# Kernel tuning notes

Measured on AMD Instinct MI355X. Metric: run time of the kernel, lower is better.

## Reference

```python
import jax, jax.numpy as jnp
import numpy as np
import math

NUM_HEADS = 8
HEAD_DIM = 64
SEQ = 128
EPS = 1e-6


def _rel_pos_bucket(rel_pos, num_buckets=32, max_dist=128):
    # bidirectional T5 bucketing
    n = -rel_pos
    num_buckets //= 2  # 16
    ret = (n < 0).astype(jnp.int32) * num_buckets
    n = jnp.abs(n)
    max_exact = num_buckets // 2  # 8
    is_small = n < max_exact
    nf = jnp.maximum(n, 1).astype(jnp.float32)  # guard log(0); masked by is_small
    val_if_large = max_exact + (
        jnp.log(nf / max_exact) / math.log(max_dist / max_exact) * (num_buckets - max_exact)
    ).astype(jnp.int32)
    val_if_large = jnp.minimum(val_if_large, num_buckets - 1)
    return ret + jnp.where(is_small, n, val_if_large)


def setup_inputs() -> dict:
    key = jax.random.key(0)
    ks = jax.random.split(key, 8)
    d = 512
    return {
        "x": jax.random.randint(ks[0], (1, SEQ), 0, 32128),
        "x_len": jax.random.randint(ks[1], (1,), 64, SEQ + 1),
        "embed": jax.random.normal(ks[2], (32128, d), jnp.float32) * 0.02,
        "scale": jnp.ones((d,), jnp.float32),
        "rel_bias_w": jax.random.normal(ks[3], (NUM_HEADS, 32), jnp.float32) * 0.02,
        "qw": jax.random.normal(ks[4], (d, d), jnp.float32) * 0.02,
        "kw": jax.random.normal(ks[5], (d, d), jnp.float32) * 0.02,
        "vw": jax.random.normal(ks[6], (d, d), jnp.float32) * 0.02,
    }


def reference(x, x_len, embed, scale, rel_bias_w, qw, kw, vw):
    B, S = x.shape  # (1, 128)
    H, D = NUM_HEADS, HEAD_DIM

    # embedding gather + RMSNorm + length mask
    h = embed[x]  # [B,S,512]
    var = jnp.mean(jnp.square(h), axis=-1, keepdims=True)
    h = h * jax.lax.rsqrt(var + EPS) * scale
    mask = (jnp.arange(S) < x_len[:, None]).astype(h.dtype)  # [B,S]
    h = h * mask[..., None]

    # relative-position bias gather [H,S,S]
    pos = jnp.arange(S, dtype=jnp.int32)
    rp_bucket = _rel_pos_bucket(pos[:, None] - pos[None, :])  # [S,S]
    rel_bias = rel_bias_w[:, rp_bucket]  # [H,S,S]
    rel_bias = rel_bias + (1.0 - mask[..., None]) * -1e9  # B==1 broadcast

    def split_heads(e):
        # [B,S,512] -> [B*H,S,D]
        return e.reshape(B, S, H, D).transpose(0, 2, 1, 3).reshape(B * H, S, D)

    q = split_heads(h @ qw)
    k = split_heads(h @ kw)
    v = split_heads(h @ vw)

    attn_weights = jnp.einsum("hqd,hkd->hqk", q, k)  # [B*H,S,S]
    attn_weights = attn_weights + jnp.transpose(rel_bias, (0, 2, 1))
    attn_probs = jax.nn.softmax(attn_weights, axis=-1)
    attn_output = jnp.einsum("hqk,hkd->hqd", attn_probs, v)  # [B*H,S,D]
    return (rel_bias, attn_weights, attn_output)
```

## Files before the change

kernel.cpp:

```cpp
#include <hip/hip_runtime.h>

#define SEQL 128
#define DM   512
#define NH   8
#define HD   64
#define MAGIC 0x13371337

typedef unsigned short ushort_t;
typedef unsigned int   uint_t;
typedef __attribute__((ext_vector_type(8))) __bf16 bf16x8;
typedef __attribute__((ext_vector_type(4))) float  f32x4;

__device__ __forceinline__ ushort_t f2bf(float f) {
    uint_t u = __float_as_uint(f);
    u += 0x7fffu + ((u >> 16) & 1u);
    return (ushort_t)(u >> 16);
}

__device__ __forceinline__ int bucket_of_delta(int d) {
    int n = d;
    int ret = 0;
    if (n < 0) { ret = 16; n = -n; }
    if (n < 8) return ret + n;
    float nf = (float)n;
    int vil = 8 + (int)((logf(nf * 0.125f) / logf(16.0f)) * 8.0f);
    vil = vil < 15 ? vil : 15;
    return ret + vil;
}

__global__ __launch_bounds__(256) void k_all(
    const int* __restrict__ x, const int* __restrict__ xlen,
    const float* __restrict__ embed, const float* __restrict__ scale,
    const float* __restrict__ rbw,
    const float* __restrict__ qw, const float* __restrict__ kw,
    const float* __restrict__ vw,
    float* __restrict__ q, float* __restrict__ k, float* __restrict__ v,
    int* __restrict__ flags,
    float* __restrict__ relb, float* __restrict__ aw, float* __restrict__ ao) {
    __shared__ char smem[49152];
    const int b = blockIdx.x, t = threadIdx.x;
    const int xl = xlen[0];

    if (b < 96) {
        ushort_t* Ash = (ushort_t*)smem;
        ushort_t* Bsh = (ushort_t*)(smem + 32768);
        const int xb = b & 7, yb = (b >> 3) & 3, zb = b >> 5;
        const int n0 = xb * 64, m0 = yb * 32;
        const float* __restrict__ W = (zb == 0) ? qw : (zb == 1) ? kw : vw;
        float* __restrict__ O       = (zb == 0) ? q  : (zb == 1) ? k  : v;

        const int nloc = t & 63, khq = t >> 6;
        const float* __restrict__ wcol = W + n0 + nloc;
        float rc[16];
#pragma unroll
        for (int i = 0; i < 16; ++i) rc[i] = wcol[(size_t)(khq * 16 + i) * DM];

        const int lane7 = t & 7, mloc = t >> 3;
        const int m = m0 + mloc;
        const int tok = x[m];
        const float4* er4 = reinterpret_cast<const float4*>(embed + (size_t)tok * DM);
        float4 va[8], vb8[8];
#pragma unroll
        for (int j = 0; j < 8; ++j) {
            va[j]  = er4[lane7 * 2 + j * 16];
            vb8[j] = er4[lane7 * 2 + j * 16 + 1];
        }
        float ss = 0.0f;
#pragma unroll
        for (int j = 0; j < 8; ++j) {
            ss += va[j].x * va[j].x + va[j].y * va[j].y + va[j].z * va[j].z + va[j].w * va[j].w;
            ss += vb8[j].x * vb8[j].x + vb8[j].y * vb8[j].y + vb8[j].z * vb8[j].z + vb8[j].w * vb8[j].w;
        }
        ss += __shfl_xor(ss, 1);
        ss += __shfl_xor(ss, 2);
        ss += __shfl_xor(ss, 4);
        float inv = rsqrtf(ss * (1.0f / DM) + 1e-6f);
        if (m >= xl) inv = 0.0f;
        const float4* sc4 = reinterpret_cast<const float4*>(scale);
#pragma unroll
        for (int j = 0; j < 8; ++j) {
            const int c = lane7 + 8 * j;
            const float4 s0 = sc4[c * 2];
            const float4 s1 = sc4[c * 2 + 1];
            ushort_t u[8];
            u[0] = f2bf(va[j].x * inv * s0.x);  u[1] = f2bf(va[j].y * inv * s0.y);
            u[2] = f2bf(va[j].z * inv * s0.z);  u[3] = f2bf(va[j].w * inv * s0.w);
            u[4] = f2bf(vb8[j].x * inv * s1.x); u[5] = f2bf(vb8[j].y * inv * s1.y);
            u[6] = f2bf(vb8[j].z * inv * s1.z); u[7] = f2bf(vb8[j].w * inv * s1.w);
            *reinterpret_cast<uint4*>((char*)Ash + mloc * 1024 + ((c ^ (mloc & 7)) << 4)) =
                *reinterpret_cast<const uint4*>(u);
        }

        {
            ushort_t u[16];
#pragma unroll
            for (int i = 0; i < 16; ++i) u[i] = f2bf(rc[i]);
            char* base = (char*)Bsh + nloc * 128;
            *reinterpret_cast<uint4*>(base + (((khq * 2 + 0) ^ (nloc & 7)) << 4)) =
                *reinterpret_cast<const uint4*>(&u[0]);
            *reinterpret_cast<uint4*>(base + (((khq * 2 + 1) ^ (nloc & 7)) << 4)) =
                *reinterpret_cast<const uint4*>(&u[8]);
        }
#pragma unroll
        for (int i = 0; i < 16; ++i) rc[i] = wcol[(size_t)(64 + khq * 16 + i) * DM];
        __syncthreads();

        const int wn = t >> 6, lane = t & 63;
        const int g = lane >> 4, l15 = lane & 15;
        f32x4 acc[2] = {};

#pragma unroll
        for (int it = 0; it < 8; ++it) {
            bf16x8 af[2][2], bfr[2];
#pragma unroll
            for (int fm = 0; fm < 2; ++fm) {
                const int ml = fm * 16 + l15;
#pragma unroll
                for (int kh = 0; kh < 2; ++kh) {
                    const int c = it * 8 + kh * 4 + g;
                    af[fm][kh] = *reinterpret_cast<const bf16x8*>(
                        (const char*)Ash + ml * 1024 + ((c ^ (ml & 7)) << 4));
                }
            }
            {
                const int nl = wn * 16 + l15;
#pragma unroll
                for (int kh = 0; kh < 2; ++kh) {
                    const int c = kh * 4 + g;
                    bfr[kh] = *reinterpret_cast<const bf16x8*>(
                        (const char*)Bsh + (it & 1) * 8192 + nl * 128 + ((c ^ (nl & 7)) << 4));
                }
            }
#pragma unroll
            for (int kh = 0; kh < 2; ++kh)
#pragma unroll
                for (int fm = 0; fm < 2; ++fm)
                    acc[fm] = __builtin_amdgcn_mfma_f32_16x16x32_bf16(
                        af[fm][kh], bfr[kh], acc[fm], 0, 0, 0);

            if (it < 7) {
                ushort_t u[16];
#pragma unroll
                for (int i = 0; i < 16; ++i) u[i] = f2bf(rc[i]);
                char* base = (char*)Bsh + ((it + 1) & 1) * 8192 + nloc * 128;
                *reinterpret_cast<uint4*>(base + (((khq * 2 + 0) ^ (nloc & 7)) << 4)) =
                    *reinterpret_cast<const uint4*>(&u[0]);
                *reinterpret_cast<uint4*>(base + (((khq * 2 + 1) ^ (nloc & 7)) << 4)) =
                    *reinterpret_cast<const uint4*>(&u[8]);
                if (it < 6) {
#pragma unroll
                    for (int i = 0; i < 16; ++i)
                        rc[i] = wcol[(size_t)((it + 2) * 64 + khq * 16 + i) * DM];
                }
            }
            __syncthreads();
        }

        {
            const int nn = n0 + wn * 16 + l15;
            float* od = O + ((size_t)(nn >> 6) * SEQL) * HD + (nn & 63);
#pragma unroll
            for (int fm = 0; fm < 2; ++fm)
#pragma unroll
                for (int r = 0; r < 4; ++r) {
                    const int mm = m0 + fm * 16 + g * 4 + r;
                    od[(size_t)mm * HD] = acc[fm][r];
                }
        }
        __syncthreads();
        if (t == 0)
            __hip_atomic_store(&flags[b], MAGIC, __ATOMIC_RELEASE,
                               __HIP_MEMORY_SCOPE_AGENT);
    } else if (b < 352) {
        float (*Ks)[HD + 4] = (float(*)[HD + 4])smem;
        float (*ps)[SEQL]   = (float(*)[SEQL])(smem + 34816);
        float* tbl          = (float*)(smem + 36864);
        const int a = b - 96, hh = a >> 5, q0 = (a & 31) * 4;

        if (t < 255) tbl[t] = rbw[hh * 32 + bucket_of_delta(t - 127)];

        if (t < 9) {
            const int fi = (t == 0) ? ((q0 >> 5) * 8 + hh)
                         : (t < 5)  ? (32 + (t - 1) * 8 + hh)
                                    : (64 + (t - 5) * 8 + hh);
            while (__hip_atomic_load(&flags[fi], __ATOMIC_RELAXED,
                                     __HIP_MEMORY_SCOPE_AGENT) != MAGIC)
                __builtin_amdgcn_s_sleep(2);
        }
        __syncthreads();
        if (t == 0)
            (void)__hip_atomic_load(&flags[0], __ATOMIC_ACQUIRE,
                                    __HIP_MEMORY_SCOPE_AGENT);
        __syncthreads();

        const float* __restrict__ kb = k + (size_t)hh * SEQL * HD;
        const float* __restrict__ vb = v + (size_t)hh * SEQL * HD;
        const float4* kb4 = reinterpret_cast<const float4*>(kb);
#pragma unroll
        for (int i = 0; i < 8; ++i) {
            const int e4 = t + i * 256;
            *reinterpret_cast<float4*>(&Ks[e4 >> 4][(e4 & 15) * 4]) = kb4[e4];
        }
        const int w = t >> 6, lane = t & 63;
        const int qi = q0 + w;
        const float4* qrow4 = reinterpret_cast<const float4*>(q + (size_t)(hh * SEQL + qi) * HD);
        float4 qr[16];
#pragma unroll
        for (int i = 0; i < 16; ++i) qr[i] = qrow4[i];
        __syncthreads();

        float lg[2];
#pragma unroll
        for (int p = 0; p < 2; ++p) {
            const int kk = lane + p * 64;
            float acc = 0.0f;
#pragma unroll
            for (int d4 = 0; d4 < 16; ++d4) {
                const float4 kv = *reinterpret_cast<const float4*>(&Ks[kk][d4 * 4]);
                acc += qr[d4].x * kv.x + qr[d4].y * kv.y + qr[d4].z * kv.z + qr[d4].w * kv.w;
            }
            float bias = tbl[qi - kk + 127];
            if (kk >= xl) bias += -1e9f;
            acc += bias;
            lg[p] = acc;
            aw[(size_t)hh * SEQL * SEQL + qi * SEQL + kk] = acc;
        }
        float mx = fmaxf(lg[0], lg[1]);
#pragma unroll
        for (int o = 32; o > 0; o >>= 1) mx = fmaxf(mx, __shfl_xor(mx, o));
        const float e0 = expf(lg[0] - mx);
        const float e1 = expf(lg[1] - mx);
        float sm = e0 + e1;
#pragma unroll
        for (int o = 32; o > 0; o >>= 1) sm += __shfl_xor(sm, o);
        const float inv = 1.0f / sm;
        ps[w][lane]      = e0 * inv;
        ps[w][lane + 64] = e1 * inv;
        float accv = 0.0f;
#pragma unroll 8
        for (int kk4 = 0; kk4 < 32; ++kk4) {
            const float4 p4 = *reinterpret_cast<const float4*>(&ps[w][kk4 * 4]);
            accv += p4.x * vb[(kk4 * 4 + 0) * HD + lane]
                  + p4.y * vb[(kk4 * 4 + 1) * HD + lane]
                  + p4.z * vb[(kk4 * 4 + 2) * HD + lane]
                  + p4.w * vb[(kk4 * 4 + 3) * HD + lane];
        }
        ao[(size_t)(hh * SEQL + qi) * HD + lane] = accv;
    } else {
        float* tbl = (float*)smem;
        const int r = b - 352, hh = r & 7, half = r >> 3;
        if (t < 255) tbl[t] = rbw[hh * 32 + bucket_of_delta(t - 127)];
        __syncthreads();
        const int qi = t & 127, kkoff = t >> 7;
#pragma unroll
        for (int j = 0; j < 32; ++j) {
            const int kk = half * 64 + j * 2 + kkoff;
            float bias = tbl[qi - kk + 127];
            if (kk >= xl) bias += -1e9f;
            relb[(size_t)hh * SEQL * SEQL + kk * SEQL + qi] = bias;
        }
    }
}

extern "C" void kernel_launch(void* const* d_in, const int* in_sizes, int n_in,
                              void* d_out, int out_size, void* d_ws, size_t ws_size,
                              hipStream_t stream) {
    const int*   x     = (const int*)d_in[0];
    const int*   xlen  = (const int*)d_in[1];
    const float* embed = (const float*)d_in[2];
    const float* scale = (const float*)d_in[3];
    const float* rbw   = (const float*)d_in[4];
    const float* qw    = (const float*)d_in[5];
    const float* kw    = (const float*)d_in[6];
    const float* vw    = (const float*)d_in[7];

    float* out  = (float*)d_out;
    float* relb = out;
    float* aw   = out + NH * SEQL * SEQL;
    float* ao   = out + 2 * NH * SEQL * SEQL;

    float* ws = (float*)d_ws;
    float* q  = ws;
    float* k  = q + SEQL * DM;
    float* v  = k + SEQL * DM;
    int* flags = (int*)(v + SEQL * DM);

    k_all<<<368, 256, 0, stream>>>(x, xlen, embed, scale, rbw, qw, kw, vw,
                                   q, k, v, flags, relb, aw, ao);
}
```

Measured before the change: 17.90 us.

## Deepen GEMM K-step, defer V-flag wait, split dot-product accumulators

The projection GEMM now stages 128-wide K chunks instead of 64, halving the number of barrier-separated iterations at the cost of more registers and a larger shared buffer. Attention blocks now wait only for the Q and K projection flags before computing logits and softmax, and wait for the V flags just before the PV product, so score work overlaps the V projection. The QK and PV dot products use four independent accumulators to shorten dependency chains. Risks are higher register pressure (32 prefetched weights) and the larger 64KB shared allocation lowering occupancy.

```diff
diff --git a/kernel.cpp b/kernel.cpp
--- a/kernel.cpp
+++ b/kernel.cpp
@@ -37,7 +37,7 @@
     float* __restrict__ q, float* __restrict__ k, float* __restrict__ v,
     int* __restrict__ flags,
     float* __restrict__ relb, float* __restrict__ aw, float* __restrict__ ao) {
-    __shared__ char smem[49152];
+    __shared__ char smem[65536];
     const int b = blockIdx.x, t = threadIdx.x;
     const int xl = xlen[0];
 
@@ -51,9 +51,9 @@
 
         const int nloc = t & 63, khq = t >> 6;
         const float* __restrict__ wcol = W + n0 + nloc;
-        float rc[16];
-#pragma unroll
-        for (int i = 0; i < 16; ++i) rc[i] = wcol[(size_t)(khq * 16 + i) * DM];
+        float rc[32];
+#pragma unroll
+        for (int i = 0; i < 32; ++i) rc[i] = wcol[(size_t)(khq * 32 + i) * DM];
 
         const int lane7 = t & 7, mloc = t >> 3;
         const int m = m0 + mloc;
@@ -92,17 +92,17 @@
         }
 
         {
-            ushort_t u[16];
-#pragma unroll
-            for (int i = 0; i < 16; ++i) u[i] = f2bf(rc[i]);
-            char* base = (char*)Bsh + nloc * 128;
-            *reinterpret_cast<uint4*>(base + (((khq * 2 + 0) ^ (nloc & 7)) << 4)) =
-                *reinterpret_cast<const uint4*>(&u[0]);
-            *reinterpret_cast<uint4*>(base + (((khq * 2 + 1) ^ (nloc & 7)) << 4)) =
-                *reinterpret_cast<const uint4*>(&u[8]);
-        }
-#pragma unroll
-        for (int i = 0; i < 16; ++i) rc[i] = wcol[(size_t)(64 + khq * 16 + i) * DM];
+            ushort_t u[32];
+#pragma unroll
+            for (int i = 0; i < 32; ++i) u[i] = f2bf(rc[i]);
+            char* base = (char*)Bsh + nloc * 256;
+#pragma unroll
+            for (int j = 0; j < 4; ++j)
+                *reinterpret_cast<uint4*>(base + (((khq * 4 + j) ^ (nloc & 7)) << 4)) =
+                    *reinterpret_cast<const uint4*>(&u[j * 8]);
+        }
+#pragma unroll
+        for (int i = 0; i < 32; ++i) rc[i] = wcol[(size_t)(128 + khq * 32 + i) * DM];
         __syncthreads();
 
         const int wn = t >> 6, lane = t & 63;
@@ -110,47 +110,35 @@
         f32x4 acc[2] = {};
 
 #pragma unroll
-        for (int it = 0; it < 8; ++it) {
-            bf16x8 af[2][2], bfr[2];
-#pragma unroll
-            for (int fm = 0; fm < 2; ++fm) {
-                const int ml = fm * 16 + l15;
-#pragma unroll
-                for (int kh = 0; kh < 2; ++kh) {
-                    const int c = it * 8 + kh * 4 + g;
-                    af[fm][kh] = *reinterpret_cast<const bf16x8*>(
-                        (const char*)Ash + ml * 1024 + ((c ^ (ml & 7)) << 4));
-                }
+        for (int it = 0; it < 4; ++it) {
+            const char* bb = (const char*)Bsh + (it & 1) * 16384;
+            const int nl  = wn * 16 + l15;
+            const int ml0 = l15, ml1 = 16 + l15;
+#pragma unroll
+            for (int kh = 0; kh < 4; ++kh) {
+                const bf16x8 bf_ = *reinterpret_cast<const bf16x8*>(
+                    bb + nl * 256 + (((kh * 4 + g) ^ (nl & 7)) << 4));
+                const int c = it * 16 + kh * 4 + g;
+                const bf16x8 a0 = *reinterpret_cast<const bf16x8*>(
+                    (const char*)Ash + ml0 * 1024 + ((c ^ (ml0 & 7)) << 4));
+                const bf16x8 a1 = *reinterpret_cast<const bf16x8*>(
+                    (const char*)Ash + ml1 * 1024 + ((c ^ (ml1 & 7)) << 4));
+                acc[0] = __builtin_amdgcn_mfma_f32_16x16x32_bf16(a0, bf_, acc[0], 0, 0, 0);
+                acc[1] = __builtin_amdgcn_mfma_f32_16x16x32_bf16(a1, bf_, acc[1], 0, 0, 0);
             }
-            {
-                const int nl = wn * 16 + l15;
-#pragma unroll
-                for (int kh = 0; kh < 2; ++kh) {
-                    const int c = kh * 4 + g;
-                    bfr[kh] = *reinterpret_cast<const bf16x8*>(
-                        (const char*)Bsh + (it & 1) * 8192 + nl * 128 + ((c ^ (nl & 7)) << 4));
-                }
-            }
-#pragma unroll
-            for (int kh = 0; kh < 2; ++kh)
-#pragma unroll
-                for (int fm = 0; fm < 2; ++fm)
-                    acc[fm] = __builtin_amdgcn_mfma_f32_16x16x32_bf16(
-                        af[fm][kh], bfr[kh], acc[fm], 0, 0, 0);
-
-            if (it < 7) {
-                ushort_t u[16];
-#pragma unroll
-                for (int i = 0; i < 16; ++i) u[i] = f2bf(rc[i]);
-                char* base = (char*)Bsh + ((it + 1) & 1) * 8192 + nloc * 128;
-                *reinterpret_cast<uint4*>(base + (((khq * 2 + 0) ^ (nloc & 7)) << 4)) =
-                    *reinterpret_cast<const uint4*>(&u[0]);
-                *reinterpret_cast<uint4*>(base + (((khq * 2 + 1) ^ (nloc & 7)) << 4)) =
-                    *reinterpret_cast<const uint4*>(&u[8]);
-                if (it < 6) {
-#pragma unroll
-                    for (int i = 0; i < 16; ++i)
-                        rc[i] = wcol[(size_t)((it + 2) * 64 + khq * 16 + i) * DM];
+            if (it < 3) {
+                ushort_t u[32];
+#pragma unroll
+                for (int i = 0; i < 32; ++i) u[i] = f2bf(rc[i]);
+                char* base = (char*)Bsh + ((it + 1) & 1) * 16384 + nloc * 256;
+#pragma unroll
+                for (int j = 0; j < 4; ++j)
+                    *reinterpret_cast<uint4*>(base + (((khq * 4 + j) ^ (nloc & 7)) << 4)) =
+                        *reinterpret_cast<const uint4*>(&u[j * 8]);
+                if (it < 2) {
+#pragma unroll
+                    for (int i = 0; i < 32; ++i)
+                        rc[i] = wcol[(size_t)((it + 2) * 128 + khq * 32 + i) * DM];
                 }
             }
             __syncthreads();
@@ -179,10 +167,8 @@
 
         if (t < 255) tbl[t] = rbw[hh * 32 + bucket_of_delta(t - 127)];
 
-        if (t < 9) {
-            const int fi = (t == 0) ? ((q0 >> 5) * 8 + hh)
-                         : (t < 5)  ? (32 + (t - 1) * 8 + hh)
-                                    : (64 + (t - 5) * 8 + hh);
+        if (t < 5) {
+            const int fi = (t == 0) ? ((q0 >> 5) * 8 + hh) : (32 + (t - 1) * 8 + hh);
             while (__hip_atomic_load(&flags[fi], __ATOMIC_RELAXED,
                                      __HIP_MEMORY_SCOPE_AGENT) != MAGIC)
                 __builtin_amdgcn_s_sleep(2);
@@ -213,12 +199,19 @@
 #pragma unroll
         for (int p = 0; p < 2; ++p) {
             const int kk = lane + p * 64;
-            float acc = 0.0f;
-#pragma unroll
-            for (int d4 = 0; d4 < 16; ++d4) {
-                const float4 kv = *reinterpret_cast<const float4*>(&Ks[kk][d4 * 4]);
-                acc += qr[d4].x * kv.x + qr[d4].y * kv.y + qr[d4].z * kv.z + qr[d4].w * kv.w;
+            float a0 = 0.0f, a1 = 0.0f, a2 = 0.0f, a3 = 0.0f;
+#pragma unroll
+            for (int d4 = 0; d4 < 16; d4 += 4) {
+                const float4 k0 = *reinterpret_cast<const float4*>(&Ks[kk][(d4 + 0) * 4]);
+                const float4 k1 = *reinterpret_cast<const float4*>(&Ks[kk][(d4 + 1) * 4]);
+                const float4 k2 = *reinterpret_cast<const float4*>(&Ks[kk][(d4 + 2) * 4]);
+                const float4 k3 = *reinterpret_cast<const float4*>(&Ks[kk][(d4 + 3) * 4]);
+                a0 += qr[d4+0].x*k0.x + qr[d4+0].y*k0.y + qr[d4+0].z*k0.z + qr[d4+0].w*k0.w;
+                a1 += qr[d4+1].x*k1.x + qr[d4+1].y*k1.y + qr[d4+1].z*k1.z + qr[d4+1].w*k1.w;
+                a2 += qr[d4+2].x*k2.x + qr[d4+2].y*k2.y + qr[d4+2].z*k2.z + qr[d4+2].w*k2.w;
+                a3 += qr[d4+3].x*k3.x + qr[d4+3].y*k3.y + qr[d4+3].z*k3.z + qr[d4+3].w*k3.w;
             }
+            float acc = (a0 + a1) + (a2 + a3);
             float bias = tbl[qi - kk + 127];
             if (kk >= xl) bias += -1e9f;
             acc += bias;
@@ -236,16 +229,36 @@
         const float inv = 1.0f / sm;
         ps[w][lane]      = e0 * inv;
         ps[w][lane + 64] = e1 * inv;
-        float accv = 0.0f;
-#pragma unroll 8
-        for (int kk4 = 0; kk4 < 32; ++kk4) {
-            const float4 p4 = *reinterpret_cast<const float4*>(&ps[w][kk4 * 4]);
-            accv += p4.x * vb[(kk4 * 4 + 0) * HD + lane]
-                  + p4.y * vb[(kk4 * 4 + 1) * HD + lane]
-                  + p4.z * vb[(kk4 * 4 + 2) * HD + lane]
-                  + p4.w * vb[(kk4 * 4 + 3) * HD + lane];
-        }
-        ao[(size_t)(hh * SEQL + qi) * HD + lane] = accv;
+
+        if (t < 4) {
+            const int fi = 64 + t * 8 + hh;
+            while (__hip_atomic_load(&flags[fi], __ATOMIC_RELAXED,
+                                     __HIP_MEMORY_SCOPE_AGENT) != MAGIC)
+                __builtin_amdgcn_s_sleep(2);
+        }
+        __syncthreads();
+        if (t == 0)
+            (void)__hip_atomic_load(&flags[64], __ATOMIC_ACQUIRE,
+                                    __HIP_MEMORY_SCOPE_AGENT);
+        __syncthreads();
+
+        float v0 = 0.0f, v1 = 0.0f, v2 = 0.0f, v3 = 0.0f;
+#pragma unroll
+        for (int kk4 = 0; kk4 < 32; kk4 += 4) {
+            const float4 p0 = *reinterpret_cast<const float4*>(&ps[w][(kk4 + 0) * 4]);
+            const float4 p1 = *reinterpret_cast<const float4*>(&ps[w][(kk4 + 1) * 4]);
+            const float4 p2 = *reinterpret_cast<const float4*>(&ps[w][(kk4 + 2) * 4]);
+            const float4 p3 = *reinterpret_cast<const float4*>(&ps[w][(kk4 + 3) * 4]);
+            v0 += p0.x * vb[((kk4+0)*4+0)*HD+lane] + p0.y * vb[((kk4+0)*4+1)*HD+lane]
+                + p0.z * vb[((kk4+0)*4+2)*HD+lane] + p0.w * vb[((kk4+0)*4+3)*HD+lane];
+            v1 += p1.x * vb[((kk4+1)*4+0)*HD+lane] + p1.y * vb[((kk4+1)*4+1)*HD+lane]
+                + p1.z * vb[((kk4+1)*4+2)*HD+lane] + p1.w * vb[((kk4+1)*4+3)*HD+lane];
+            v2 += p2.x * vb[((kk4+2)*4+0)*HD+lane] + p2.y * vb[((kk4+2)*4+1)*HD+lane]
+                + p2.z * vb[((kk4+2)*4+2)*HD+lane] + p2.w * vb[((kk4+2)*4+3)*HD+lane];
+            v3 += p3.x * vb[((kk4+3)*4+0)*HD+lane] + p3.y * vb[((kk4+3)*4+1)*HD+lane]
+                + p3.z * vb[((kk4+3)*4+2)*HD+lane] + p3.w * vb[((kk4+3)*4+3)*HD+lane];
+        }
+        ao[(size_t)(hh * SEQL + qi) * HD + lane] = (v0 + v1) + (v2 + v3);
     } else {
         float* tbl = (float*)smem;
         const int r = b - 352, hh = r & 7, half = r >> 3;
```

New measurement: 18.59 us. 3.9% more time.
